# Kernel tuning notes

Measured on AMD Instinct MI355X. Metric: run time of the kernel, lower is better.

Reference implementation:

```python
import jax, jax.numpy as jnp
import numpy as np

N_E, E_DIM = 2048, 256
B, H, W = 32, 32, 32


def setup_inputs() -> dict:
    key = jax.random.key(0)
    k1, k2 = jax.random.split(key)
    z = jax.random.normal(k1, (B, E_DIM, H, W), dtype=jnp.float32)
    embedding = jax.random.normal(k2, (N_E, E_DIM), dtype=jnp.float32)
    return {"z": z, "embedding": embedding}


def reference(z, embedding):
    # z: [B, C, H, W] with C == e_dim; embedding: [n_e, e_dim]
    n_e, e_dim = embedding.shape
    b, c, h, w = z.shape
    z_nhwc = jnp.transpose(z, (0, 2, 3, 1))            # [B,H,W,C]
    z_flat = z_nhwc.reshape(-1, e_dim)                 # [L, D]
    # squared euclidean distance: ||z||^2 + ||e||^2 - 2 z.e^T
    d = (
        jnp.sum(z_flat * z_flat, axis=1, keepdims=True)
        + jnp.sum(embedding * embedding, axis=1)
        - 2.0 * jnp.einsum("ld,nd->ln", z_flat, embedding)
    )                                                  # [L, n_e]
    idx = jnp.argmin(d, axis=1)                        # [L]
    z_q = jnp.take(embedding, idx, axis=0).reshape(b, h, w, e_dim)
    # embed_ema=True -> commitment-only loss (codebook updated by EMA, not grads)
    loss = jnp.mean((jax.lax.stop_gradient(z_q) - z_nhwc) ** 2)
    # straight-through estimator
    z_q_st = z_nhwc + jax.lax.stop_gradient(z_q - z_nhwc)
    quantize = jnp.transpose(z_q_st, (0, 3, 1, 2))     # [B,C,H,W]
    # number of distinct codebook entries used (jit-safe via scatter-set)
    used = jnp.sum(jnp.zeros((n_e,), z.dtype).at[idx].set(1.0))
    index = idx.reshape(b, h, w)
    return quantize, loss, index, used
```

## Files before the change

### kernel.cpp

```cpp
#include <hip/hip_runtime.h>
#include <cfloat>

#define Dm 256
#define HW 1024
#define NE 2048
#define L_TOT 32768
#define QOFF 8388608
#define TAU 0.1f

#define QSCALE 4064.0f
#define CHC 7.93613e-3f
#define CXC 3.10005e-5f

typedef __attribute__((ext_vector_type(4))) int i32x4;
typedef const __attribute__((address_space(1))) unsigned int* as1_u32p;
typedef __attribute__((address_space(3))) unsigned int* as3_u32p;

#define GLL(gp, lp) __builtin_amdgcn_global_load_lds((as1_u32p)(gp), (as3_u32p)(lp), 16, 0, 0)

__device__ __forceinline__ void q8(float x, signed char& hi, signed char& lo) {
    int xi = __float2int_rn(x * QSCALE);
    xi = max(-32512, min(32512, xi));
    int h = (xi + 128) >> 8;
    hi = (signed char)h;
    lo = (signed char)(xi - (h << 8));
}

__global__ void k_enorm(const float* __restrict__ emb, float* __restrict__ enorm) {
    int w = threadIdx.x >> 6, lane = threadIdx.x & 63;
    int n = blockIdx.x * 4 + w;
    const float4 v = *reinterpret_cast<const float4*>(emb + (size_t)n * Dm + lane * 4);
    double s = (double)v.x * v.x + (double)v.y * v.y + (double)v.z * v.z + (double)v.w * v.w;
    #pragma unroll
    for (int off = 32; off; off >>= 1) s += __shfl_xor(s, off);
    if (lane == 0) enorm[n] = (float)s;
}

__global__ __launch_bounds__(256) void k_split_i8(
    const float* __restrict__ z, const float* __restrict__ emb,
    signed char* __restrict__ z_hi, signed char* __restrict__ z_lo,
    signed char* __restrict__ e_hi, signed char* __restrict__ e_lo,
    float* __restrict__ enorm, float* __restrict__ zn_part,
    float* __restrict__ used, int* __restrict__ flag_cnt)
{
    __shared__ signed char zh[32][264];
    __shared__ signed char zl[32][264];
    __shared__ double zsum[4];
    const int t = threadIdx.x;
    const int w = t >> 6, lane = t & 63;

    if (blockIdx.x >= 16 && blockIdx.x < 24) used[(blockIdx.x - 16) * 256 + t] = 0.f;
    if (blockIdx.x == 24 && t == 0) *flag_cnt = 0;

    if (w < 2) {
        int n = blockIdx.x * 2 + w;
        const float4 v = *reinterpret_cast<const float4*>(emb + (size_t)n * Dm + lane * 4);
        float vv[4] = { v.x, v.y, v.z, v.w };
        double s = (double)v.x * v.x + (double)v.y * v.y + (double)v.z * v.z + (double)v.w * v.w;
        #pragma unroll
        for (int off = 32; off; off >>= 1) s += __shfl_xor(s, off);
        if (lane == 0) enorm[n] = (float)s;
        signed char h4[4], l4[4];
        #pragma unroll
        for (int j = 0; j < 4; ++j) q8(vv[j], h4[j], l4[j]);
        *reinterpret_cast<int*>(e_hi + (size_t)n * Dm + lane * 4) = *reinterpret_cast<int*>(h4);
        *reinterpret_cast<int*>(e_lo + (size_t)n * Dm + lane * 4) = *reinterpret_cast<int*>(l4);
    }

    const int b  = blockIdx.x >> 5;
    const int p0 = (blockIdx.x & 31) * 32;
    const int pp = t & 31, cb = t >> 5;
    const float* zb = z + (size_t)b * (Dm * HW) + p0 + pp;
    float zs = 0.f;
    for (int ci = 0; ci < 32; ++ci) {
        int c = ci * 8 + cb;
        float x = zb[(size_t)c * HW];
        zs = fmaf(x, x, zs);
        q8(x, zh[pp][c], zl[pp][c]);
    }
    double d = zs;
    #pragma unroll
    for (int off = 32; off; off >>= 1) d += __shfl_xor(d, off);
    if ((t & 63) == 0) zsum[w] = d;
    __syncthreads();
    if (t == 0) zn_part[blockIdx.x] = (float)(zsum[0] + zsum[1] + zsum[2] + zsum[3]);
    const int l0 = b * 1024 + p0;
    #pragma unroll
    for (int r = 0; r < 8; ++r) {
        int id = r * 256 + t;
        int row = id >> 6, ch = id & 63;
        *reinterpret_cast<int*>(z_hi + (size_t)(l0 + row) * Dm + ch * 4) =
            *reinterpret_cast<int*>(&zh[row][ch * 4]);
        *reinterpret_cast<int*>(z_lo + (size_t)(l0 + row) * Dm + ch * 4) =
            *reinterpret_cast<int*>(&zl[row][ch * 4]);
    }
}

__global__ __launch_bounds__(256, 2) void k_score_i8(
    const signed char* __restrict__ zh, const signed char* __restrict__ zl,
    const signed char* __restrict__ eh, const signed char* __restrict__ el,
    const float* __restrict__ enorm,
    float* __restrict__ pd1, float* __restrict__ pd2, int* __restrict__ pi1)
{
    __shared__ signed char ldsA[2][16384];
    __shared__ signed char ldsB[2][16384];

    const int t    = threadIdx.x;
    const int lane = t & 63, w = t >> 6;
    const int wm = w >> 1, wc = w & 1;
    const int c15 = lane & 15, g4 = lane >> 4;

    const int bx = blockIdx.x;
    const int wg = (bx & 7) * 64 + (bx >> 3);
    const int mi = wg >> 1, ni = wg & 1;
    const int l0 = mi * 128;
    const int nbase = ni * 1024;

    const int srow = t & 127;
    const int cb0  = t >> 7;
    unsigned aoffs[4], boffs[4];
    #pragma unroll
    for (int r = 0; r < 4; ++r) {
        aoffs[r] = (unsigned)((l0 + srow) * Dm + (cb0 + 2 * r) * 16);
        boffs[r] = (unsigned)((nbase + srow) * Dm + (cb0 + 2 * r) * 16);
    }
    const int ldd = t * 16;

    int offA[4], offB[4];
    #pragma unroll
    for (int m = 0; m < 4; ++m) offA[m] = g4 * 2048 + (wm * 64 + m * 16 + c15) * 16;
    #pragma unroll
    for (int n = 0; n < 4; ++n) offB[n] = g4 * 2048 + (wc * 64 + n * 16 + c15) * 16;

    float d1[4][4], d2[4][4]; int i1[4][4];
    #pragma unroll
    for (int m = 0; m < 4; ++m)
        #pragma unroll
        for (int r = 0; r < 4; ++r) { d1[m][r] = 3.4e38f; d2[m][r] = 3.4e38f; i1[m][r] = 0; }

    #pragma unroll
    for (int r = 0; r < 4; ++r) {
        GLL(zh + aoffs[r], &ldsA[0][ldd + r * 4096]);
        GLL(eh + boffs[r], &ldsB[0][ldd + r * 4096]);
    }
    __syncthreads();

    int cur = 0, it = 0;
    int pnt = 0, pkt = 1;
    unsigned pntoff = 0;

    auto kstep = [&](i32x4 (&ACC)[4][4]) {
        if (it + 1 < 48) {
            const int term = pkt >> 1;
            const unsigned kcf = (unsigned)((pkt & 1) << 7);
            const signed char* As = (term == 2) ? zl : zh;
            const signed char* Bs = (term == 1) ? el : eh;
            #pragma unroll
            for (int r = 0; r < 4; ++r) {
                GLL(As + aoffs[r] + kcf,          &ldsA[cur ^ 1][ldd + r * 4096]);
                GLL(Bs + boffs[r] + pntoff + kcf, &ldsB[cur ^ 1][ldd + r * 4096]);
            }
            if (++pkt == 6) { pkt = 0; ++pnt; pntoff = (unsigned)pnt << 15; }
        }
        #pragma unroll
        for (int ks = 0; ks < 2; ++ks) {
            i32x4 af[4], bfv[4];
            #pragma unroll
            for (int m = 0; m < 4; ++m)
                af[m] = *reinterpret_cast<const i32x4*>(&ldsA[cur][ks * 8192 + offA[m]]);
            #pragma unroll
            for (int n = 0; n < 4; ++n)
                bfv[n] = *reinterpret_cast<const i32x4*>(&ldsB[cur][ks * 8192 + offB[n]]);
            __builtin_amdgcn_s_setprio(1);
            #pragma unroll
            for (int m = 0; m < 4; ++m)
                #pragma unroll
                for (int n = 0; n < 4; ++n)
                    ACC[m][n] = __builtin_amdgcn_mfma_i32_16x16x64_i8(
                        af[m], bfv[n], ACC[m][n], 0, 0, 0);
            __builtin_amdgcn_s_setprio(0);
        }
        __syncthreads();
        cur ^= 1;
        ++it;
    };

    for (int nt = 0; nt < 8; ++nt) {
        i32x4 accH[4][4], accX[4][4];
        #pragma unroll
        for (int m = 0; m < 4; ++m)
            #pragma unroll
            for (int n = 0; n < 4; ++n) {
                accH[m][n] = (i32x4){0, 0, 0, 0};
                accX[m][n] = (i32x4){0, 0, 0, 0};
            }

        kstep(accH); kstep(accH);
        kstep(accX); kstep(accX);
        kstep(accX); kstep(accX);

        int n0 = nbase + nt * 128;
        #pragma unroll
        for (int n = 0; n < 4; ++n) {
            int ng = n0 + wc * 64 + n * 16 + c15;
            float en = enorm[ng];
            #pragma unroll
            for (int m = 0; m < 4; ++m)
                #pragma unroll
                for (int r = 0; r < 4; ++r) {
                    float sx = fmaf(-CXC, (float)accX[m][n][r], en);
                    float s  = fmaf(-CHC, (float)accH[m][n][r], sx);
                    if (s < d1[m][r]) { d2[m][r] = d1[m][r]; d1[m][r] = s; i1[m][r] = ng; }
                    else if (s < d2[m][r]) d2[m][r] = s;
                }
        }
    }

    #pragma unroll
    for (int off = 1; off <= 8; off <<= 1) {
        #pragma unroll
        for (int m = 0; m < 4; ++m)
            #pragma unroll
            for (int r = 0; r < 4; ++r) {
                float od1 = __shfl_xor(d1[m][r], off);
                int   oi1 = __shfl_xor(i1[m][r], off);
                float od2 = __shfl_xor(d2[m][r], off);
                float nd2 = fminf(fminf(d2[m][r], od2), fmaxf(d1[m][r], od1));
                if (od1 < d1[m][r] || (od1 == d1[m][r] && oi1 < i1[m][r])) {
                    d1[m][r] = od1; i1[m][r] = oi1;
                }
                d2[m][r] = nd2;
            }
    }

    float* rs1 = (float*)&ldsA[0][0];
    float* rs2 = rs1 + 128;
    int*   ri  = (int*)(rs2 + 128);
    if (wc == 1 && c15 == 0) {
        #pragma unroll
        for (int m = 0; m < 4; ++m)
            #pragma unroll
            for (int r = 0; r < 4; ++r) {
                int q = wm * 64 + m * 16 + g4 * 4 + r;
                rs1[q] = d1[m][r];
                rs2[q] = d2[m][r];
                ri [q] = i1[m][r];
            }
    }
    __syncthreads();
    if (wc == 0 && c15 == 0) {
        #pragma unroll
        for (int m = 0; m < 4; ++m)
            #pragma unroll
            for (int r = 0; r < 4; ++r) {
                int q = wm * 64 + m * 16 + g4 * 4 + r;
                float bd1 = d1[m][r], bd2 = d2[m][r]; int bi1 = i1[m][r];
                float od1 = rs1[q], od2 = rs2[q];
                int   oi1 = ri [q];
                float nd2 = fminf(fminf(bd2, od2), fmaxf(bd1, od1));
                if (od1 < bd1 || (od1 == bd1 && oi1 < bi1)) { bd1 = od1; bi1 = oi1; }
                bd2 = nd2;
                int gq = l0 + q;
                pd1[ni * L_TOT + gq] = bd1;
                pd2[ni * L_TOT + gq] = bd2;
                pi1[ni * L_TOT + gq] = bi1;
            }
    }
}

__global__ __launch_bounds__(256) void k_mg(
    const float* __restrict__ pd1, const float* __restrict__ pd2,
    const int* __restrict__ pi1, const float* __restrict__ emb,
    int* __restrict__ ws_idx, float* __restrict__ out_idxf,
    float* __restrict__ used, int* __restrict__ flag_cnt,
    int* __restrict__ flag_list, float* __restrict__ d1_part,
    float* __restrict__ outq)
{
    __shared__ int sidx[64];
    __shared__ float eldT[Dm][65];
    const int t = threadIdx.x;
    const int l0 = blockIdx.x * 64;
    const int b = l0 >> 10, p0 = l0 & 1023;

    if (t < 64) {
        int gq = l0 + t;
        float d1 = pd1[gq], d2 = pd2[gq]; int i1 = pi1[gq];
        float od1 = pd1[L_TOT + gq], od2 = pd2[L_TOT + gq];
        int   oi1 = pi1[L_TOT + gq];
        float nd2 = fminf(fminf(d2, od2), fmaxf(d1, od1));
        if (od1 < d1 || (od1 == d1 && oi1 < i1)) { d1 = od1; i1 = oi1; }
        d2 = nd2;
        ws_idx[gq] = i1;
        out_idxf[gq] = (float)i1;
        if (d2 - d1 < TAU) {
            int pos = atomicAdd(flag_cnt, 1);
            flag_list[pos] = gq;
        } else {
            used[i1] = 1.0f;
        }
        sidx[t] = i1;
        float s = d1;
        #pragma unroll
        for (int off = 32; off; off >>= 1) s += __shfl_xor(s, off);
        if (t == 0) d1_part[blockIdx.x] = s;
    }
    __syncthreads();

    int w = t >> 6, lane = t & 63;
    for (int r = 0; r < 16; ++r) {
        int q = r * 4 + w;
        const float4 v = *reinterpret_cast<const float4*>(emb + (size_t)sidx[q] * Dm + lane * 4);
        eldT[lane * 4 + 0][q] = v.x; eldT[lane * 4 + 1][q] = v.y;
        eldT[lane * 4 + 2][q] = v.z; eldT[lane * 4 + 3][q] = v.w;
    }
    __syncthreads();
    const size_t obase = (size_t)b * (Dm * HW) + p0 + lane;
    #pragma unroll 4
    for (int it = 0; it < 64; ++it) {
        int c = w * 64 + it;
        outq[obase + (size_t)c * HW] = eldT[c][lane];
    }
}

#define BM 64
#define BN 128
#define BK 64
__global__ __launch_bounds__(256, 2) void k_argmin_f32(
    const float* __restrict__ z, const float* __restrict__ emb,
    const float* __restrict__ enorm, int* __restrict__ ws_idx,
    float* __restrict__ out_idxf, float* __restrict__ used,
    int* __restrict__ flag_cnt, int* __restrict__ flag_list)
{
    __shared__ float zlds[BK][BM];
    __shared__ float el[BK][BN + 4];
    __shared__ float rd1[4][64];
    __shared__ int   ri1[4][64];
    __shared__ float rd2[4][64];

    const int t  = threadIdx.x;
    const int tq = t & 15;
    const int tn = t >> 4;
    const int l0 = blockIdx.x * BM;
    const int b  = l0 >> 10, p0 = l0 & 1023;
    const float* zb = z + (size_t)b * (Dm * HW) + p0;

    float d1[4], d2[4]; int i1[4];
    #pragma unroll
    for (int i = 0; i < 4; ++i) { d1[i] = FLT_MAX; d2[i] = FLT_MAX; i1[i] = 0; }

    for (int nt = 0; nt < NE / BN; ++nt) {
        const int n0 = nt * BN;
        float acc[4][8];
        #pragma unroll
        for (int i = 0; i < 4; ++i)
            #pragma unroll
            for (int j = 0; j < 8; ++j) acc[i][j] = 0.f;

        for (int kc = 0; kc < Dm / BK; ++kc) {
            __syncthreads();
            #pragma unroll
            for (int r = 0; r < 4; ++r) {
                int f = r * 256 + t;
                int kk = f >> 4, q4 = (f & 15) << 2;
                float4 v = *reinterpret_cast<const float4*>(zb + (size_t)(kc * BK + kk) * HW + q4);
                *reinterpret_cast<float4*>(&zlds[kk][q4]) = v;
            }
            #pragma unroll
            for (int r = 0; r < 8; ++r) {
                int f = r * 256 + t;
                int n = f >> 4, k4 = (f & 15) << 2;
                float4 v = *reinterpret_cast<const float4*>(emb + (size_t)(n0 + n) * Dm + kc * BK + k4);
                el[k4 + 0][n] = v.x; el[k4 + 1][n] = v.y;
                el[k4 + 2][n] = v.z; el[k4 + 3][n] = v.w;
            }
            __syncthreads();
            #pragma unroll 4
            for (int kk = 0; kk < BK; ++kk) {
                float4 zf = *reinterpret_cast<const float4*>(&zlds[kk][tq << 2]);
                float4 e0 = *reinterpret_cast<const float4*>(&el[kk][tn << 3]);
                float4 e1 = *reinterpret_cast<const float4*>(&el[kk][(tn << 3) + 4]);
                float zr[4] = { zf.x, zf.y, zf.z, zf.w };
                float er[8] = { e0.x, e0.y, e0.z, e0.w, e1.x, e1.y, e1.z, e1.w };
                #pragma unroll
                for (int i = 0; i < 4; ++i)
                    #pragma unroll
                    for (int j = 0; j < 8; ++j)
                        acc[i][j] = fmaf(zr[i], er[j], acc[i][j]);
            }
        }
        #pragma unroll
        for (int j = 0; j < 8; ++j) {
            int ng = n0 + (tn << 3) + j;
            float en = enorm[ng];
            #pragma unroll
            for (int i = 0; i < 4; ++i) {
                float s = fmaf(-2.f, acc[i][j], en);
                if (s < d1[i]) { d2[i] = d1[i]; d1[i] = s; i1[i] = ng; }
                else if (s < d2[i]) d2[i] = s;
            }
        }
    }
    #pragma unroll
    for (int off = 16; off <= 32; off <<= 1) {
        #pragma unroll
        for (int i = 0; i < 4; ++i) {
            float od1 = __shfl_xor(d1[i], off);
            int   oi1 = __shfl_xor(i1[i], off);
            float od2 = __shfl_xor(d2[i], off);
            float nd2 = fminf(fminf(d2[i], od2), fmaxf(d1[i], od1));
            bool take = (od1 < d1[i]) || (od1 == d1[i] && oi1 < i1[i]);
            if (take) { d1[i] = od1; i1[i] = oi1; }
            d2[i] = nd2;
        }
    }
    int w = t >> 6;
    if ((t & 63) < 16) {
        #pragma unroll
        for (int i = 0; i < 4; ++i) {
            rd1[w][(tq << 2) + i] = d1[i];
            ri1[w][(tq << 2) + i] = i1[i];
            rd2[w][(tq << 2) + i] = d2[i];
        }
    }
    __syncthreads();
    if (t < 64) {
        float bd1 = rd1[0][t]; int bi1 = ri1[0][t]; float bd2 = rd2[0][t];
        #pragma unroll
        for (int ww = 1; ww < 4; ++ww) {
            float od1 = rd1[ww][t]; int oi1 = ri1[ww][t]; float od2 = rd2[ww][t];
            float nd2 = fminf(fminf(bd2, od2), fmaxf(bd1, od1));
            if (od1 < bd1 || (od1 == bd1 && oi1 < bi1)) { bd1 = od1; bi1 = oi1; }
            bd2 = nd2;
        }
        int l = l0 + t;
        ws_idx[l] = bi1;
        out_idxf[l] = (float)bi1;
        if (bd2 - bd1 < TAU) {
            int pos = atomicAdd(flag_cnt, 1);
            flag_list[pos] = l;
        } else {
            used[bi1] = 1.0f;
        }
    }
}

__global__ __launch_bounds__(256) void k_refine_scan(
    const float* __restrict__ z, const float* __restrict__ emb,
    const int* __restrict__ flag_cnt, const int* __restrict__ flag_list,
    double* __restrict__ pbd, int* __restrict__ pbi)
{
    __shared__ float zrow[Dm];
    __shared__ double sd[256];
    __shared__ int    si[256];
    const int t = threadIdx.x;
    const int ntask = *flag_cnt * 8;
    for (int task = blockIdx.x; task < ntask; task += gridDim.x) {
        const int fi = task >> 3, chunk = task & 7;
        const int l = flag_list[fi];
        const int b = l >> 10, p = l & 1023;
        const float* zq = z + (size_t)b * (Dm * HW) + p;
        __syncthreads();
        zrow[t] = zq[(size_t)t * HW];
        __syncthreads();
        const int n = chunk * 256 + t;
        const float* er = emb + (size_t)n * Dm;
        double dt0 = 0.0, dt1 = 0.0, dt2 = 0.0, dt3 = 0.0;
        double nm0 = 0.0, nm1 = 0.0, nm2 = 0.0, nm3 = 0.0;
        for (int c = 0; c < Dm; c += 4) {
            double e0 = er[c], e1 = er[c + 1], e2 = er[c + 2], e3 = er[c + 3];
            dt0 += e0 * (double)zrow[c];     nm0 += e0 * e0;
            dt1 += e1 * (double)zrow[c + 1]; nm1 += e1 * e1;
            dt2 += e2 * (double)zrow[c + 2]; nm2 += e2 * e2;
            dt3 += e3 * (double)zrow[c + 3]; nm3 += e3 * e3;
        }
        sd[t] = (nm0 + nm1) + (nm2 + nm3) - 2.0 * ((dt0 + dt1) + (dt2 + dt3));
        si[t] = n;
        __syncthreads();
        for (int st = 128; st; st >>= 1) {
            if (t < st) {
                double od = sd[t + st]; int oi = si[t + st];
                if (od < sd[t] || (od == sd[t] && oi < si[t])) { sd[t] = od; si[t] = oi; }
            }
            __syncthreads();
        }
        if (t == 0) { pbd[task] = sd[0]; pbi[task] = si[0]; }
    }
}

__global__ __launch_bounds__(256) void k_refine_merge(
    const float* __restrict__ emb, const int* __restrict__ flag_cnt,
    const int* __restrict__ flag_list, const double* __restrict__ pbd,
    const int* __restrict__ pbi, int* __restrict__ ws_idx,
    float* __restrict__ out_idxf, float* __restrict__ used,
    float* __restrict__ outq)
{
    __shared__ int bestn;
    const int t = threadIdx.x;
    const int nf = *flag_cnt;
    for (int fi = blockIdx.x; fi < nf; fi += gridDim.x) {
        const int l = flag_list[fi];
        __syncthreads();
        if (t == 0) {
            double bd = pbd[fi * 8]; int bi = pbi[fi * 8];
            #pragma unroll
            for (int c = 1; c < 8; ++c) {
                double od = pbd[fi * 8 + c]; int oi = pbi[fi * 8 + c];
                if (od < bd || (od == bd && oi < bi)) { bd = od; bi = oi; }
            }
            ws_idx[l] = bi;
            out_idxf[l] = (float)bi;
            used[bi] = 1.0f;
            bestn = bi;
        }
        __syncthreads();
        const int b = l >> 10, p = l & 1023;
        outq[(size_t)b * (Dm * HW) + (size_t)t * HW + p] = emb[(size_t)bestn * Dm + t];
    }
}

__global__ void k_refine(const float* __restrict__ z, const float* __restrict__ emb,
                         const int* __restrict__ flag_cnt, const int* __restrict__ flag_list,
                         int* __restrict__ ws_idx, float* __restrict__ out_idxf,
                         float* __restrict__ used, float* __restrict__ outq)
{
    __shared__ float zrow[Dm];
    __shared__ double sd[256];
    __shared__ int    si[256];
    int nf = *flag_cnt;
    for (int fi = blockIdx.x; fi < nf; fi += gridDim.x) {
        int l = flag_list[fi];
        int b = l >> 10, p = l & 1023;
        const float* zq = z + (size_t)b * (Dm * HW) + p;
        __syncthreads();
        for (int c = threadIdx.x; c < Dm; c += blockDim.x) zrow[c] = zq[(size_t)c * HW];
        __syncthreads();
        double bd = DBL_MAX; int bi = 0;
        for (int nb = 0; nb < NE / 256; ++nb) {
            int n = nb * 256 + threadIdx.x;
            const float* er = emb + (size_t)n * Dm;
            double dt0 = 0.0, dt1 = 0.0, dt2 = 0.0, dt3 = 0.0;
            double nm0 = 0.0, nm1 = 0.0, nm2 = 0.0, nm3 = 0.0;
            for (int c = 0; c < Dm; c += 4) {
                double e0 = er[c], e1 = er[c + 1], e2 = er[c + 2], e3 = er[c + 3];
                dt0 += e0 * (double)zrow[c];     nm0 += e0 * e0;
                dt1 += e1 * (double)zrow[c + 1]; nm1 += e1 * e1;
                dt2 += e2 * (double)zrow[c + 2]; nm2 += e2 * e2;
                dt3 += e3 * (double)zrow[c + 3]; nm3 += e3 * e3;
            }
            double s = (nm0 + nm1) + (nm2 + nm3) - 2.0 * ((dt0 + dt1) + (dt2 + dt3));
            if (s < bd) { bd = s; bi = n; }
        }
        sd[threadIdx.x] = bd; si[threadIdx.x] = bi;
        __syncthreads();
        for (int st = 128; st; st >>= 1) {
            if (threadIdx.x < (unsigned)st) {
                double od = sd[threadIdx.x + st]; int oi = si[threadIdx.x + st];
                if (od < sd[threadIdx.x] || (od == sd[threadIdx.x] && oi < si[threadIdx.x])) {
                    sd[threadIdx.x] = od; si[threadIdx.x] = oi;
                }
            }
            __syncthreads();
        }
        if (threadIdx.x == 0) {
            ws_idx[l] = si[0];
            out_idxf[l] = (float)si[0];
            used[si[0]] = 1.0f;
        }
        __syncthreads();
        int bi0 = si[0];
        int c = threadIdx.x;
        outq[(size_t)b * (Dm * HW) + (size_t)c * HW + p] = emb[(size_t)bi0 * Dm + c];
        __syncthreads();
    }
}

__global__ __launch_bounds__(256) void k_gather_loss(
    const float* __restrict__ z, const float* __restrict__ emb,
    const int* __restrict__ ws_idx, float* __restrict__ outq,
    float* __restrict__ partials)
{
    __shared__ int sidx[64];
    __shared__ float eldT[Dm][65];
    __shared__ float wsum[4];
    const int t = threadIdx.x;
    const int l0 = blockIdx.x * 64;
    const int b = l0 >> 10, p0 = l0 & 1023;
    if (t < 64) sidx[t] = ws_idx[l0 + t];
    __syncthreads();
    int w = t >> 6, lane = t & 63;
    for (int r = 0; r < 16; ++r) {
        int q = r * 4 + w;
        const float4 v = *reinterpret_cast<const float4*>(emb + (size_t)sidx[q] * Dm + lane * 4);
        eldT[lane * 4 + 0][q] = v.x; eldT[lane * 4 + 1][q] = v.y;
        eldT[lane * 4 + 2][q] = v.z; eldT[lane * 4 + 3][q] = v.w;
    }
    __syncthreads();
    float ls = 0.f;
    const size_t obase = (size_t)b * (Dm * HW) + p0 + lane;
    for (int it = 0; it < 64; ++it) {
        int c = w * 64 + it;
        size_t o = obase + (size_t)c * HW;
        float qv = eldT[c][lane];
        float zv = z[o];
        outq[o] = qv;
        float df = qv - zv;
        ls = fmaf(df, df, ls);
    }
    #pragma unroll
    for (int off = 32; off; off >>= 1) ls += __shfl_xor(ls, off);
    if (lane == 0) wsum[w] = ls;
    __syncthreads();
    if (t == 0) partials[blockIdx.x] = wsum[0] + wsum[1] + wsum[2] + wsum[3];
}

__global__ void k_final(const float* __restrict__ zn_part, const float* __restrict__ d1_part,
                        int nd1, const float* __restrict__ used,
                        float* __restrict__ out_loss, float* __restrict__ out_used)
{
    __shared__ double s1[256];
    __shared__ float  s2[256];
    int t = threadIdx.x;
    double a = 0.0;
    for (int i = t; i < 1024; i += 256) a += (double)zn_part[i];
    for (int i = t; i < nd1; i += 256) a += (double)d1_part[i];
    float u = 0.f;
    for (int i = t; i < NE; i += 256) u += used[i];
    s1[t] = a; s2[t] = u;
    __syncthreads();
    for (int st = 128; st; st >>= 1) {
        if (t < st) { s1[t] += s1[t + st]; s2[t] += s2[t + st]; }
        __syncthreads();
    }
    if (t == 0) { *out_loss = (float)(s1[0] / 8388608.0); *out_used = s2[0]; }
}

__global__ void k_final_fb(const float* __restrict__ partials, const float* __restrict__ used,
                           float* __restrict__ out_loss, float* __restrict__ out_used)
{
    __shared__ float s1[256], s2[256];
    int t = threadIdx.x;
    float a = partials[t] + partials[t + 256];
    float u = 0.f;
    for (int i = t; i < NE; i += 256) u += used[i];
    s1[t] = a; s2[t] = u;
    __syncthreads();
    for (int st = 128; st; st >>= 1) {
        if (t < st) { s1[t] += s1[t + st]; s2[t] += s2[t + st]; }
        __syncthreads();
    }
    if (t == 0) { *out_loss = s1[0] / 8388608.f; *out_used = s2[0]; }
}

extern "C" void kernel_launch(void* const* d_in, const int* in_sizes, int n_in,
                              void* d_out, int out_size, void* d_ws, size_t ws_size,
                              hipStream_t stream) {
    const float* z   = (const float*)d_in[0];
    const float* emb = (const float*)d_in[1];
    float* out      = (float*)d_out;
    float* outq     = out;
    float* out_loss = out + QOFF;
    float* out_idxf = out + QOFF + 1;
    float* out_used = out + QOFF + 1 + L_TOT;

    float* ws       = (float*)d_ws;
    float* enorm    = ws;
    float* used     = ws + 2048;
    float* zn_part  = ws + 4096;
    float* d1_part  = ws + 5120;
    int*   flag_cnt = (int*)(ws + 5632);
    int*   ws_idx   = (int*)(ws + 5888);
    int*   flag_list= (int*)(ws + 5888 + L_TOT);

    float* pd1w = ws + 71680;
    float* pd2w = ws + 137216;
    int*   pi1w = (int*)(ws + 202752);

    size_t i8_bytes = 2ull * (NE + L_TOT) * Dm;
    size_t pbd_off_f = 268288 + i8_bytes / 4;
    size_t pbi_off_f = pbd_off_f + 2 * 262144;
    size_t need_i8 = (pbi_off_f + 262144) * 4;

    if (ws_size >= need_i8) {
        signed char* e_hi8 = (signed char*)(ws + 268288);
        signed char* e_lo8 = e_hi8 + (size_t)NE * Dm;
        signed char* z_hi8 = e_lo8 + (size_t)NE * Dm;
        signed char* z_lo8 = z_hi8 + (size_t)L_TOT * Dm;
        double* pbd = (double*)(ws + pbd_off_f);
        int*    pbi = (int*)(ws + pbi_off_f);
        k_split_i8<<<1024, 256, 0, stream>>>(z, emb, z_hi8, z_lo8, e_hi8, e_lo8,
                                             enorm, zn_part, used, flag_cnt);
        k_score_i8<<<512, 256, 0, stream>>>(z_hi8, z_lo8, e_hi8, e_lo8, enorm,
                                            pd1w, pd2w, pi1w);
        k_mg<<<L_TOT / 64, 256, 0, stream>>>(pd1w, pd2w, pi1w, emb, ws_idx, out_idxf,
                                             used, flag_cnt, flag_list, d1_part, outq);
        k_refine_scan<<<2048, 256, 0, stream>>>(z, emb, flag_cnt, flag_list, pbd, pbi);
        k_refine_merge<<<256, 256, 0, stream>>>(emb, flag_cnt, flag_list, pbd, pbi,
                                                ws_idx, out_idxf, used, outq);
        k_final<<<1, 256, 0, stream>>>(zn_part, d1_part, 512, used, out_loss, out_used);
    } else {
        hipMemsetAsync(used, 0, (size_t)3584 * 4, stream);
        k_enorm<<<NE / 4, 256, 0, stream>>>(emb, enorm);
        k_argmin_f32<<<L_TOT / BM, 256, 0, stream>>>(z, emb, enorm, ws_idx, out_idxf, used,
                                                     flag_cnt, flag_list);
        k_refine<<<256, 256, 0, stream>>>(z, emb, flag_cnt, flag_list, ws_idx, out_idxf,
                                          used, outq);
        k_gather_loss<<<L_TOT / 64, 256, 0, stream>>>(z, emb, ws_idx, outq, zn_part);
        k_final_fb<<<1, 256, 0, stream>>>(zn_part, used, out_loss, out_used);
    }
}
```

Baseline: 243.1 us.

## Keep full A tile resident in LDS and stream B in K=64 chunks

The score kernel now loads the block's whole 128-row hi/lo z tile (64KB) into LDS once, instead of reloading A slices for every codebook tile. Only the embedding hi/lo chunks are double-buffered, in 8KB K=64 steps, with the hi·hi and lo·hi products sharing each B fragment load. This cuts repeated global/L2 traffic for A. In exchange it uses more LDS per block (about 80KB, which is tight for two blocks per CU), needs more barriers per tile, and the el steps issue only 16 MFMAs per barrier, which may hide latency less well.

Measured after the change: 216.7 us. 10.8% less time.

```diff
diff --git a/kernel.cpp b/kernel.cpp
--- a/kernel.cpp
+++ b/kernel.cpp
@@ -102,8 +102,8 @@
     const float* __restrict__ enorm,
     float* __restrict__ pd1, float* __restrict__ pd2, int* __restrict__ pi1)
 {
-    __shared__ signed char ldsA[2][16384];
-    __shared__ signed char ldsB[2][16384];
+    __shared__ signed char ldsA[65536];
+    __shared__ signed char ldsB[2][8192];
 
     const int t    = threadIdx.x;
     const int lane = t & 63, w = t >> 6;
@@ -117,18 +117,31 @@
     const int nbase = ni * 1024;
 
     const int srow = t & 127;
-    const int cb0  = t >> 7;
-    unsigned aoffs[4], boffs[4];
-    #pragma unroll
-    for (int r = 0; r < 4; ++r) {
-        aoffs[r] = (unsigned)((l0 + srow) * Dm + (cb0 + 2 * r) * 16);
-        boffs[r] = (unsigned)((nbase + srow) * Dm + (cb0 + 2 * r) * 16);
-    }
+    const int sc16 = t >> 7;
+    const unsigned abase = (unsigned)((l0 + srow) * Dm);
+    const unsigned bbase = (unsigned)((nbase + srow) * Dm);
     const int ldd = t * 16;
 
-    int offA[4], offB[4];
-    #pragma unroll
-    for (int m = 0; m < 4; ++m) offA[m] = g4 * 2048 + (wm * 64 + m * 16 + c15) * 16;
+    #pragma unroll
+    for (int arr = 0; arr < 2; ++arr) {
+        const signed char* As = arr ? zl : zh;
+        #pragma unroll
+        for (int kc = 0; kc < 4; ++kc) {
+            #pragma unroll
+            for (int r = 0; r < 2; ++r) {
+                GLL(As + abase + kc * 64 + (r * 2 + sc16) * 16,
+                    &ldsA[((arr * 4 + kc) * 2 + r) * 4096 + ldd]);
+            }
+        }
+    }
+    #pragma unroll
+    for (int r = 0; r < 2; ++r)
+        GLL(eh + bbase + (r * 2 + sc16) * 16, &ldsB[0][r * 4096 + ldd]);
+    __syncthreads();
+
+    int rowA[4], offB[4];
+    #pragma unroll
+    for (int m = 0; m < 4; ++m) rowA[m] = g4 * 2048 + (wm * 64 + m * 16 + c15) * 16;
     #pragma unroll
     for (int n = 0; n < 4; ++n) offB[n] = g4 * 2048 + (wc * 64 + n * 16 + c15) * 16;
 
@@ -138,53 +151,7 @@
         #pragma unroll
         for (int r = 0; r < 4; ++r) { d1[m][r] = 3.4e38f; d2[m][r] = 3.4e38f; i1[m][r] = 0; }
 
-    #pragma unroll
-    for (int r = 0; r < 4; ++r) {
-        GLL(zh + aoffs[r], &ldsA[0][ldd + r * 4096]);
-        GLL(eh + boffs[r], &ldsB[0][ldd + r * 4096]);
-    }
-    __syncthreads();
-
-    int cur = 0, it = 0;
-    int pnt = 0, pkt = 1;
-    unsigned pntoff = 0;
-
-    auto kstep = [&](i32x4 (&ACC)[4][4]) {
-        if (it + 1 < 48) {
-            const int term = pkt >> 1;
-            const unsigned kcf = (unsigned)((pkt & 1) << 7);
-            const signed char* As = (term == 2) ? zl : zh;
-            const signed char* Bs = (term == 1) ? el : eh;
-            #pragma unroll
-            for (int r = 0; r < 4; ++r) {
-                GLL(As + aoffs[r] + kcf,          &ldsA[cur ^ 1][ldd + r * 4096]);
-                GLL(Bs + boffs[r] + pntoff + kcf, &ldsB[cur ^ 1][ldd + r * 4096]);
-            }
-            if (++pkt == 6) { pkt = 0; ++pnt; pntoff = (unsigned)pnt << 15; }
-        }
-        #pragma unroll
-        for (int ks = 0; ks < 2; ++ks) {
-            i32x4 af[4], bfv[4];
-            #pragma unroll
-            for (int m = 0; m < 4; ++m)
-                af[m] = *reinterpret_cast<const i32x4*>(&ldsA[cur][ks * 8192 + offA[m]]);
-            #pragma unroll
-            for (int n = 0; n < 4; ++n)
-                bfv[n] = *reinterpret_cast<const i32x4*>(&ldsB[cur][ks * 8192 + offB[n]]);
-            __builtin_amdgcn_s_setprio(1);
-            #pragma unroll
-            for (int m = 0; m < 4; ++m)
-                #pragma unroll
-                for (int n = 0; n < 4; ++n)
-                    ACC[m][n] = __builtin_amdgcn_mfma_i32_16x16x64_i8(
-                        af[m], bfv[n], ACC[m][n], 0, 0, 0);
-            __builtin_amdgcn_s_setprio(0);
-        }
-        __syncthreads();
-        cur ^= 1;
-        ++it;
-    };
-
+    int cur = 0;
     for (int nt = 0; nt < 8; ++nt) {
         i32x4 accH[4][4], accX[4][4];
         #pragma unroll
@@ -195,9 +162,57 @@
                 accX[m][n] = (i32x4){0, 0, 0, 0};
             }
 
-        kstep(accH); kstep(accH);
-        kstep(accX); kstep(accX);
-        kstep(accX); kstep(accX);
+        #pragma unroll
+        for (int c = 0; c < 8; ++c) {
+            if (!(c == 7 && nt == 7)) {
+                int nc = c + 1, nnt = nt;
+                if (nc == 8) { nc = 0; ++nnt; }
+                const signed char* Bs = (nc < 4) ? eh : el;
+                const unsigned boff = bbase + ((unsigned)nnt << 15) + (unsigned)((nc & 3) * 64);
+                #pragma unroll
+                for (int r = 0; r < 2; ++r)
+                    GLL(Bs + boff + (r * 2 + sc16) * 16, &ldsB[cur ^ 1][r * 4096 + ldd]);
+            }
+            const int kc = c & 3;
+            i32x4 bfv[4];
+            #pragma unroll
+            for (int n = 0; n < 4; ++n)
+                bfv[n] = *reinterpret_cast<const i32x4*>(&ldsB[cur][offB[n]]);
+            if (c < 4) {
+                i32x4 afh[4], afl[4];
+                #pragma unroll
+                for (int m = 0; m < 4; ++m) {
+                    afh[m] = *reinterpret_cast<const i32x4*>(&ldsA[kc * 8192 + rowA[m]]);
+                    afl[m] = *reinterpret_cast<const i32x4*>(&ldsA[(4 + kc) * 8192 + rowA[m]]);
+                }
+                __builtin_amdgcn_s_setprio(1);
+                #pragma unroll
+                for (int m = 0; m < 4; ++m)
+                    #pragma unroll
+                    for (int n = 0; n < 4; ++n) {
+                        accH[m][n] = __builtin_amdgcn_mfma_i32_16x16x64_i8(
+                            afh[m], bfv[n], accH[m][n], 0, 0, 0);
+                        accX[m][n] = __builtin_amdgcn_mfma_i32_16x16x64_i8(
+                            afl[m], bfv[n], accX[m][n], 0, 0, 0);
+                    }
+                __builtin_amdgcn_s_setprio(0);
+            } else {
+                i32x4 afh[4];
+                #pragma unroll
+                for (int m = 0; m < 4; ++m)
+                    afh[m] = *reinterpret_cast<const i32x4*>(&ldsA[kc * 8192 + rowA[m]]);
+                __builtin_amdgcn_s_setprio(1);
+                #pragma unroll
+                for (int m = 0; m < 4; ++m)
+                    #pragma unroll
+                    for (int n = 0; n < 4; ++n)
+                        accX[m][n] = __builtin_amdgcn_mfma_i32_16x16x64_i8(
+                            afh[m], bfv[n], accX[m][n], 0, 0, 0);
+                __builtin_amdgcn_s_setprio(0);
+            }
+            __syncthreads();
+            cur ^= 1;
+        }
 
         int n0 = nbase + nt * 128;
         #pragma unroll
@@ -233,7 +248,7 @@
             }
     }
 
-    float* rs1 = (float*)&ldsA[0][0];
+    float* rs1 = (float*)&ldsA[0];
     float* rs2 = rs1 + 128;
     int*   ri  = (int*)(rs2 + 128);
     if (wc == 1 && c15 == 0) {
```
